# Kernel tuning notes

Measured on AMD Instinct MI355X. Metric: run time of the kernel, lower is better.

The kernel has to match this reference:

```python
import jax, jax.numpy as jnp
import numpy as np

DIM = 384
NUM_HEADS = 6
HEAD_DIM = DIM // NUM_HEADS
SCALE = HEAD_DIM ** -0.5


def setup_inputs() -> dict:
    key = jax.random.key(0)
    k_x, k_wqkv, k_bqkv, k_wp, k_bp = jax.random.split(key, 5)
    B, N, D = 16, 1024, DIM
    s = 0.02
    return {
        "x": jax.random.normal(k_x, (B, N, D), dtype=jnp.float32),
        "w_qkv": jax.random.normal(k_wqkv, (D, 3 * D), dtype=jnp.float32) * s,
        "b_qkv": jax.random.normal(k_bqkv, (3 * D,), dtype=jnp.float32) * s,
        "w_proj": jax.random.normal(k_wp, (D, D), dtype=jnp.float32) * s,
        "b_proj": jax.random.normal(k_bp, (D,), dtype=jnp.float32) * s,
    }


def reference(x, w_qkv, b_qkv, w_proj, b_proj):
    b, n, d = x.shape
    qkv = x @ w_qkv + b_qkv                               # (B, N, 3D)
    qkv = qkv.reshape(b, n, 3, NUM_HEADS, HEAD_DIM)
    qkv = jnp.transpose(qkv, (2, 0, 3, 1, 4))             # (3, B, H, N, hd)
    q, k, v = qkv[0], qkv[1], qkv[2]
    attn = jnp.einsum("bhqd,bhkd->bhqk", q, k) * SCALE    # (B, H, N, N)
    attn = jax.nn.softmax(attn, axis=-1)
    out = jnp.einsum("bhqk,bhkd->bhqd", attn, v)          # (B, H, N, hd)
    out = jnp.transpose(out, (0, 2, 1, 3)).reshape(b, n, d)
    return out @ w_proj + b_proj
```

## Files before the change

kernel.cpp:

```cpp
#include <hip/hip_runtime.h>

typedef __attribute__((ext_vector_type(8))) short short8;
typedef __attribute__((ext_vector_type(4))) float float4_t;
typedef __attribute__((ext_vector_type(4))) unsigned int uint4_t;

#define MFMA16(A, B, C) __builtin_amdgcn_mfma_f32_16x16x32_bf16(A, B, C, 0, 0, 0)

#define QSCALE 0.1803368801111168f

__device__ __forceinline__ unsigned short f2bf(float f) {
  unsigned int u = __builtin_bit_cast(unsigned int, f);
  u += 0x7FFFu + ((u >> 16) & 1u);
  return (unsigned short)(u >> 16);
}

__device__ __forceinline__ void gload16(const unsigned short* g, unsigned short* l) {
  __builtin_amdgcn_global_load_lds(
      (const __attribute__((address_space(1))) unsigned int*)(g),
      (__attribute__((address_space(3))) unsigned int*)(l), 16, 0, 0);
}

__global__ __launch_bounds__(256) void prep(
    const float* __restrict__ x, const float* __restrict__ w_qkv,
    const float* __restrict__ w_proj, unsigned short* __restrict__ xb,
    unsigned short* __restrict__ wqkvT, unsigned short* __restrict__ wprojT) {
  __shared__ unsigned short tile[32][33];
  const int bid = blockIdx.x, tid = threadIdx.x;
  if (bid < 6144) {
    const int i = bid * 256 + tid;
    float4 v = reinterpret_cast<const float4*>(x)[i];
    ushort4 r;
    r.x = f2bf(v.x); r.y = f2bf(v.y); r.z = f2bf(v.z); r.w = f2bf(v.w);
    reinterpret_cast<ushort4*>(xb)[i] = r;
    return;
  }
  const float* w; unsigned short* wT; int E, t;
  if (bid < 6576) { t = bid - 6144; w = w_qkv; wT = wqkvT; E = 1152; }
  else            { t = bid - 6576; w = w_proj; wT = wprojT; E = 384; }
  const int tiles_e = E >> 5;
  const int td = t / tiles_e, te = t - td * tiles_e;
  const int r = tid >> 3, c4 = (tid & 7) * 4;
  float4 v = *reinterpret_cast<const float4*>(&w[(size_t)(td * 32 + r) * E + te * 32 + c4]);
  tile[r][c4 + 0] = f2bf(v.x);
  tile[r][c4 + 1] = f2bf(v.y);
  tile[r][c4 + 2] = f2bf(v.z);
  tile[r][c4 + 3] = f2bf(v.w);
  __syncthreads();
  ushort4 o;
  o.x = tile[c4 + 0][r]; o.y = tile[c4 + 1][r];
  o.z = tile[c4 + 2][r]; o.w = tile[c4 + 3][r];
  *reinterpret_cast<ushort4*>(&wT[(size_t)(te * 32 + r) * 384 + td * 32 + c4]) = o;
}

__global__ __launch_bounds__(256, 3) void gemm_qkv(
    const unsigned short* __restrict__ xb,
    const unsigned short* __restrict__ wT,
    const float* __restrict__ bias,
    unsigned short* __restrict__ qb,
    unsigned short* __restrict__ kb,
    unsigned short* __restrict__ vt) {
  __shared__ alignas(16) char smem[49152];
  const int tid = threadIdx.x;
  const int wg = (blockIdx.x & 7) * 288 + (blockIdx.x >> 3);
  const int bm = wg / 18, bn = wg - bm * 18;
  const int m0 = bm * 128, n0 = bn * 64;
  const int lane = tid & 63, wid = tid >> 6;
  const int lr = lane & 15, lg = lane >> 4;
  const int wm = wid >> 1, wn = wid & 1;
  float4_t acc[4][2] = {};

  const unsigned short* asrc[4];
  const unsigned short* bsrc[2];
  int adst[4], bdst[2];
#pragma unroll
  for (int i = 0; i < 4; ++i) {
    const int idx = tid + i * 256;
    const int r = idx >> 3, c8 = idx & 7;
    asrc[i] = xb + (size_t)(m0 + r) * 384 + (c8 ^ (r & 7)) * 8;
    adst[i] = idx * 16;
  }
#pragma unroll
  for (int i = 0; i < 2; ++i) {
    const int idx = tid + i * 256;
    const int r = idx >> 3, c8 = idx & 7;
    bsrc[i] = wT + (size_t)(n0 + r) * 384 + (c8 ^ (r & 7)) * 8;
    bdst[i] = idx * 16;
  }
  const int rxor = (lr & 7) << 4;

#pragma unroll
  for (int i = 0; i < 4; ++i) gload16(asrc[i], (unsigned short*)(smem + adst[i]));
#pragma unroll
  for (int i = 0; i < 2; ++i) gload16(bsrc[i], (unsigned short*)(smem + 32768 + bdst[i]));
  __syncthreads();

#pragma unroll
  for (int kt = 0; kt < 6; ++kt) {
    const int cur = kt & 1;
    if (kt < 5) {
#pragma unroll
      for (int i = 0; i < 4; ++i)
        gload16(asrc[i] + (kt + 1) * 64,
                (unsigned short*)(smem + (cur ^ 1) * 16384 + adst[i]));
#pragma unroll
      for (int i = 0; i < 2; ++i)
        gload16(bsrc[i] + (kt + 1) * 64,
                (unsigned short*)(smem + 32768 + (cur ^ 1) * 8192 + bdst[i]));
    }
    const char* Ab = smem + cur * 16384;
    const char* Bb = smem + 32768 + cur * 8192;
#pragma unroll
    for (int kk = 0; kk < 2; ++kk) {
      short8 a[4], b[2];
#pragma unroll
      for (int f = 0; f < 4; ++f)
        a[f] = *reinterpret_cast<const short8*>(
            Ab + (wm * 64 + f * 16 + lr) * 128 + ((kk * 64 + lg * 16) ^ rxor));
#pragma unroll
      for (int f = 0; f < 2; ++f)
        b[f] = *reinterpret_cast<const short8*>(
            Bb + (wn * 32 + f * 16 + lr) * 128 + ((kk * 64 + lg * 16) ^ rxor));
      if (bn < 12) {
#pragma unroll
        for (int mf = 0; mf < 4; ++mf)
#pragma unroll
          for (int nf = 0; nf < 2; ++nf)
            acc[mf][nf] = MFMA16(b[nf], a[mf], acc[mf][nf]);
      } else {
#pragma unroll
        for (int mf = 0; mf < 4; ++mf)
#pragma unroll
          for (int nf = 0; nf < 2; ++nf)
            acc[mf][nf] = MFMA16(a[mf], b[nf], acc[mf][nf]);
      }
    }
    __syncthreads();
  }

  if (bn < 12) {
    const int whichk = (bn >= 6);
    unsigned short* dst = whichk ? kb : qb;
    const float sc = whichk ? 1.f : QSCALE;
#pragma unroll
    for (int nf = 0; nf < 2; ++nf) {
      const int e0 = n0 + wn * 32 + nf * 16 + lg * 4;
      const int d0 = e0 - whichk * 384;
      const int h = d0 >> 6, hi0 = d0 & 63;
      const float4 bv4 = *reinterpret_cast<const float4*>(&bias[e0]);
#pragma unroll
      for (int mf = 0; mf < 4; ++mf) {
        const int mm = m0 + wm * 64 + mf * 16 + lr;
        const int b0 = mm >> 10, n_b = mm & 1023;
        const size_t bhh = (size_t)(b0 * 6 + h);
        ushort4 sv;
        sv.x = f2bf((acc[mf][nf][0] + bv4.x) * sc);
        sv.y = f2bf((acc[mf][nf][1] + bv4.y) * sc);
        sv.z = f2bf((acc[mf][nf][2] + bv4.z) * sc);
        sv.w = f2bf((acc[mf][nf][3] + bv4.w) * sc);
        *reinterpret_cast<ushort4*>(&dst[bhh * 65536 + (size_t)n_b * 64 + hi0]) = sv;
      }
    }
  } else {
#pragma unroll
    for (int nf = 0; nf < 2; ++nf) {
      const int e = n0 + wn * 32 + nf * 16 + lr;
      const float bv = bias[e];
      const int d = e - 768;
      const int h = d >> 6, hi = d & 63;
#pragma unroll
      for (int mf = 0; mf < 4; ++mf) {
        const int mm0 = m0 + wm * 64 + mf * 16 + lg * 4;
        const int b0 = mm0 >> 10, n_b = mm0 & 1023;
        const size_t bhh = (size_t)(b0 * 6 + h);
        const int np = (n_b & ~31) | ((n_b & 12) << 1) | ((n_b & 16) >> 2);
        ushort4 sv;
        sv.x = f2bf(acc[mf][nf][0] + bv);
        sv.y = f2bf(acc[mf][nf][1] + bv);
        sv.z = f2bf(acc[mf][nf][2] + bv);
        sv.w = f2bf(acc[mf][nf][3] + bv);
        *reinterpret_cast<ushort4*>(&vt[bhh * 65536 + (size_t)hi * 1024 + np]) = sv;
      }
    }
  }
}

__global__ __launch_bounds__(512, 6) void attn(
    const unsigned short* __restrict__ qb,
    const unsigned short* __restrict__ kb,
    const unsigned short* __restrict__ vt,
    unsigned short* __restrict__ ab) {
  __shared__ alignas(16) char smem[32768];
  const int tid = threadIdx.x;
  const int wg = (blockIdx.x & 7) * 96 + (blockIdx.x >> 3);
  const int bh = wg >> 3, qt = wg & 7;
  const int lane = tid & 63, wid = tid >> 6;
  const int lr = lane & 15, lg = lane >> 4;
  const size_t base = (size_t)bh * 65536;
  const unsigned short* qp = qb + base;
  const unsigned short* kp = kb + base;
  const unsigned short* vp = vt + base;
  const int q0 = qt * 128 + wid * 16;

  short8 aq0 = *reinterpret_cast<const short8*>(&qp[(size_t)(q0 + lr) * 64 + lg * 8]);
  short8 aq1 = *reinterpret_cast<const short8*>(&qp[(size_t)(q0 + lr) * 64 + 32 + lg * 8]);

  const int rr = tid >> 3;
  const int cc = (((tid & 7) * 16) ^ ((rr & 7) << 4)) >> 1;
  const unsigned short* ksrc = kp + rr * 64 + cc;
  const unsigned short* vsrc = vp + rr * 1024 + cc;
  unsigned short* kdst = (unsigned short*)(smem + tid * 16);
  unsigned short* vdst = (unsigned short*)(smem + 16384 + tid * 16);

  const int xr = (lr & 7) << 4;

  float lsum = 0.f;
  float4_t o[4] = {};

  gload16(ksrc, kdst);
  gload16(vsrc, vdst);
  __syncthreads();

  for (int kt = 0; kt < 16; ++kt) {
    const int cur = kt & 1;
    if (kt < 15) {
      const int nb = (cur ^ 1) * 8192;
      gload16(ksrc + (kt + 1) * 4096, (unsigned short*)(smem + nb + tid * 16));
      gload16(vsrc + (kt + 1) * 64, (unsigned short*)(smem + 16384 + nb + tid * 16));
    }
    const char* kbase = smem + cur * 8192;
    const char* vbase = smem + 16384 + cur * 8192;

#pragma unroll
    for (int half = 0; half < 2; ++half) {
      short8 bk00 = *reinterpret_cast<const short8*>(
          kbase + (half * 32 + lr) * 128 + ((lg * 16) ^ xr));
      short8 bk01 = *reinterpret_cast<const short8*>(
          kbase + (half * 32 + lr) * 128 + ((64 + lg * 16) ^ xr));
      short8 bk10 = *reinterpret_cast<const short8*>(
          kbase + (half * 32 + 16 + lr) * 128 + ((lg * 16) ^ xr));
      short8 bk11 = *reinterpret_cast<const short8*>(
          kbase + (half * 32 + 16 + lr) * 128 + ((64 + lg * 16) ^ xr));
      float4_t s0 = {}, s1 = {};
      __builtin_amdgcn_s_setprio(1);
      s0 = MFMA16(bk00, aq0, s0);
      s0 = MFMA16(bk01, aq1, s0);
      s1 = MFMA16(bk10, aq0, s1);
      s1 = MFMA16(bk11, aq1, s1);
      __builtin_amdgcn_s_setprio(0);

      unsigned int dw0, dw1, dw2, dw3;
      {
        const float p0 = __builtin_amdgcn_exp2f(s0[0]);
        const float p1 = __builtin_amdgcn_exp2f(s0[1]);
        const float p2 = __builtin_amdgcn_exp2f(s0[2]);
        const float p3 = __builtin_amdgcn_exp2f(s0[3]);
        asm("v_cvt_pk_bf16_f32 %0, %1, %2" : "=v"(dw0) : "v"(p0), "v"(p1));
        asm("v_cvt_pk_bf16_f32 %0, %1, %2" : "=v"(dw1) : "v"(p2), "v"(p3));
        const float p4 = __builtin_amdgcn_exp2f(s1[0]);
        const float p5 = __builtin_amdgcn_exp2f(s1[1]);
        const float p6 = __builtin_amdgcn_exp2f(s1[2]);
        const float p7 = __builtin_amdgcn_exp2f(s1[3]);
        asm("v_cvt_pk_bf16_f32 %0, %1, %2" : "=v"(dw2) : "v"(p4), "v"(p5));
        asm("v_cvt_pk_bf16_f32 %0, %1, %2" : "=v"(dw3) : "v"(p6), "v"(p7));
      }
      const float t0 = __builtin_bit_cast(float, dw0 << 16) +
                       __builtin_bit_cast(float, dw0 & 0xFFFF0000u);
      const float t1 = __builtin_bit_cast(float, dw1 << 16) +
                       __builtin_bit_cast(float, dw1 & 0xFFFF0000u);
      const float t2 = __builtin_bit_cast(float, dw2 << 16) +
                       __builtin_bit_cast(float, dw2 & 0xFFFF0000u);
      const float t3 = __builtin_bit_cast(float, dw3 << 16) +
                       __builtin_bit_cast(float, dw3 & 0xFFFF0000u);
      lsum += (t0 + t1) + (t2 + t3);

      uint4_t pw;
      pw[0] = dw0; pw[1] = dw1; pw[2] = dw2; pw[3] = dw3;
      const short8 pa = __builtin_bit_cast(short8, pw);
      short8 bv0 = *reinterpret_cast<const short8*>(
          vbase + (0 * 16 + lr) * 128 + ((half * 64 + lg * 16) ^ xr));
      short8 bv1 = *reinterpret_cast<const short8*>(
          vbase + (1 * 16 + lr) * 128 + ((half * 64 + lg * 16) ^ xr));
      short8 bv2 = *reinterpret_cast<const short8*>(
          vbase + (2 * 16 + lr) * 128 + ((half * 64 + lg * 16) ^ xr));
      short8 bv3 = *reinterpret_cast<const short8*>(
          vbase + (3 * 16 + lr) * 128 + ((half * 64 + lg * 16) ^ xr));
      __builtin_amdgcn_s_setprio(1);
      o[0] = MFMA16(pa, bv0, o[0]);
      o[1] = MFMA16(pa, bv1, o[1]);
      o[2] = MFMA16(pa, bv2, o[2]);
      o[3] = MFMA16(pa, bv3, o[3]);
      __builtin_amdgcn_s_setprio(0);
    }
    __syncthreads();
  }

  float t = lsum;
  t += __shfl_xor(t, 16);
  t += __shfl_xor(t, 32);
  const float inv = 1.f / t;

  const int b = bh / 6, h = bh - b * 6;
  float invj[4];
#pragma unroll
  for (int j = 0; j < 4; ++j)
    invj[j] = __shfl(inv, lg * 4 + j);
#pragma unroll
  for (int f = 0; f < 4; ++f)
#pragma unroll
    for (int j = 0; j < 4; ++j) {
      const int q = q0 + lg * 4 + j;
      ab[(size_t)(b * 1024 + q) * 384 + h * 64 + f * 16 + lr] =
          f2bf(o[f][j] * invj[j]);
    }
}

__global__ __launch_bounds__(256, 3) void gemm_proj(
    const unsigned short* __restrict__ ab,
    const unsigned short* __restrict__ wT,
    const float* __restrict__ bias,
    float* __restrict__ out) {
  __shared__ alignas(16) char smem[49152];
  const int tid = threadIdx.x;
  const int wg = (blockIdx.x & 7) * 96 + (blockIdx.x >> 3);
  const int bm = wg / 3, bn = wg - bm * 3;
  const int m0 = bm * 64, n0 = bn * 128;
  const int lane = tid & 63, wid = tid >> 6;
  const int lr = lane & 15, lg = lane >> 4;
  const int wm = wid >> 1, wn = wid & 1;
  float4_t acc[2][4] = {};

  const unsigned short* asrc[2];
  const unsigned short* bsrc[4];
  int adst[2], bdst[4];
#pragma unroll
  for (int i = 0; i < 2; ++i) {
    const int idx = tid + i * 256;
    const int r = idx >> 3, c8 = idx & 7;
    asrc[i] = ab + (size_t)(m0 + r) * 384 + (c8 ^ (r & 7)) * 8;
    adst[i] = idx * 16;
  }
#pragma unroll
  for (int i = 0; i < 4; ++i) {
    const int idx = tid + i * 256;
    const int r = idx >> 3, c8 = idx & 7;
    bsrc[i] = wT + (size_t)(n0 + r) * 384 + (c8 ^ (r & 7)) * 8;
    bdst[i] = idx * 16;
  }
  const int rxor = (lr & 7) << 4;

#pragma unroll
  for (int i = 0; i < 2; ++i) gload16(asrc[i], (unsigned short*)(smem + adst[i]));
#pragma unroll
  for (int i = 0; i < 4; ++i) gload16(bsrc[i], (unsigned short*)(smem + 16384 + bdst[i]));
  __syncthreads();

#pragma unroll
  for (int kt = 0; kt < 6; ++kt) {
    const int cur = kt & 1;
    if (kt < 5) {
#pragma unroll
      for (int i = 0; i < 2; ++i)
        gload16(asrc[i] + (kt + 1) * 64, (unsigned short*)(smem + (cur ^ 1) * 8192 + adst[i]));
#pragma unroll
      for (int i = 0; i < 4; ++i)
        gload16(bsrc[i] + (kt + 1) * 64, (unsigned short*)(smem + 16384 + (cur ^ 1) * 16384 + bdst[i]));
    }
    const char* Ab = smem + cur * 8192;
    const char* Bb = smem + 16384 + cur * 16384;
#pragma unroll
    for (int kk = 0; kk < 2; ++kk) {
      short8 a[2], b[4];
#pragma unroll
      for (int f = 0; f < 2; ++f)
        a[f] = *reinterpret_cast<const short8*>(
            Ab + (wm * 32 + f * 16 + lr) * 128 + ((kk * 64 + lg * 16) ^ rxor));
#pragma unroll
      for (int f = 0; f < 4; ++f)
        b[f] = *reinterpret_cast<const short8*>(
            Bb + (wn * 64 + f * 16 + lr) * 128 + ((kk * 64 + lg * 16) ^ rxor));
#pragma unroll
      for (int mf = 0; mf < 2; ++mf)
#pragma unroll
        for (int nf = 0; nf < 4; ++nf)
          acc[mf][nf] = MFMA16(b[nf], a[mf], acc[mf][nf]);
    }
    __syncthreads();
  }

#pragma unroll
  for (int nf = 0; nf < 4; ++nf) {
    const int e0 = n0 + wn * 64 + nf * 16 + lg * 4;
    const float4 bv4 = *reinterpret_cast<const float4*>(&bias[e0]);
#pragma unroll
    for (int mf = 0; mf < 2; ++mf) {
      const int mm = m0 + wm * 32 + mf * 16 + lr;
      float4 ov;
      ov.x = acc[mf][nf][0] + bv4.x;
      ov.y = acc[mf][nf][1] + bv4.y;
      ov.z = acc[mf][nf][2] + bv4.z;
      ov.w = acc[mf][nf][3] + bv4.w;
      *reinterpret_cast<float4*>(&out[(size_t)mm * 384 + e0]) = ov;
    }
  }
}

extern "C" void kernel_launch(void* const* d_in, const int* in_sizes, int n_in,
                              void* d_out, int out_size, void* d_ws, size_t ws_size,
                              hipStream_t stream) {
  const float* x      = (const float*)d_in[0];
  const float* w_qkv  = (const float*)d_in[1];
  const float* b_qkv  = (const float*)d_in[2];
  const float* w_proj = (const float*)d_in[3];
  const float* b_proj = (const float*)d_in[4];
  float* out = (float*)d_out;

  char* ws = (char*)d_ws;
  unsigned short* xb     = (unsigned short*)(ws);
  unsigned short* wqkvT  = (unsigned short*)(ws + 12582912);
  unsigned short* wprojT = (unsigned short*)(ws + 13467648);
  unsigned short* qb     = (unsigned short*)(ws + 13762560);
  unsigned short* kb     = (unsigned short*)(ws + 26345472);
  unsigned short* vt     = (unsigned short*)(ws + 38928384);
  unsigned short* ab     = xb;

  prep<<<6720, 256, 0, stream>>>(x, w_qkv, w_proj, xb, wqkvT, wprojT);
  gemm_qkv<<<2304, 256, 0, stream>>>(xb, wqkvT, b_qkv, qb, kb, vt);
  attn<<<768, 512, 0, stream>>>(qb, kb, vt, ab);
  gemm_proj<<<768, 256, 0, stream>>>(ab, wprojT, b_proj, out);
}
```

Baseline: 88.34 us.

## Give each attention wave two query tiles so K/V LDS reads are reused

The attention kernel drops from 512 to 256 threads per block, and each wave now processes 32 query rows (two 16-row fragments) instead of 16. The K and V fragments read from LDS are reused across both query fragments, which halves LDS read traffic per unit of MFMA work. Each thread now issues two async global-to-LDS loads per tile instead of one. The cost is more registers per wave (two output accumulators, four Q fragments) and fewer waves per block, which may reduce latency hiding.

```diff
diff --git a/kernel.cpp b/kernel.cpp
--- a/kernel.cpp
+++ b/kernel.cpp
@@ -184,7 +184,7 @@
   }
 }
 
-__global__ __launch_bounds__(512, 6) void attn(
+__global__ __launch_bounds__(256, 3) void attn(
     const unsigned short* __restrict__ qb,
     const unsigned short* __restrict__ kb,
     const unsigned short* __restrict__ vt,
@@ -199,33 +199,49 @@
   const unsigned short* qp = qb + base;
   const unsigned short* kp = kb + base;
   const unsigned short* vp = vt + base;
-  const int q0 = qt * 128 + wid * 16;
-
-  short8 aq0 = *reinterpret_cast<const short8*>(&qp[(size_t)(q0 + lr) * 64 + lg * 8]);
-  short8 aq1 = *reinterpret_cast<const short8*>(&qp[(size_t)(q0 + lr) * 64 + 32 + lg * 8]);
-
-  const int rr = tid >> 3;
-  const int cc = (((tid & 7) * 16) ^ ((rr & 7) << 4)) >> 1;
-  const unsigned short* ksrc = kp + rr * 64 + cc;
-  const unsigned short* vsrc = vp + rr * 1024 + cc;
-  unsigned short* kdst = (unsigned short*)(smem + tid * 16);
-  unsigned short* vdst = (unsigned short*)(smem + 16384 + tid * 16);
-
+  const int q0 = qt * 128 + wid * 32;
+
+  short8 aq[2][2];
+#pragma unroll
+  for (int qf = 0; qf < 2; ++qf)
+#pragma unroll
+    for (int h = 0; h < 2; ++h)
+      aq[qf][h] = *reinterpret_cast<const short8*>(
+          &qp[(size_t)(q0 + qf * 16 + lr) * 64 + h * 32 + lg * 8]);
+
+  const unsigned short* ksrc[2];
+  const unsigned short* vsrc[2];
+  int soff[2];
+#pragma unroll
+  for (int i = 0; i < 2; ++i) {
+    const int idx = tid + i * 256;
+    const int r = idx >> 3, c8 = idx & 7;
+    const int cc = (c8 ^ (r & 7)) * 8;
+    ksrc[i] = kp + r * 64 + cc;
+    vsrc[i] = vp + r * 1024 + cc;
+    soff[i] = idx * 16;
+  }
   const int xr = (lr & 7) << 4;
 
-  float lsum = 0.f;
-  float4_t o[4] = {};
-
-  gload16(ksrc, kdst);
-  gload16(vsrc, vdst);
+  float lsum0 = 0.f, lsum1 = 0.f;
+  float4_t o0[4] = {}, o1[4] = {};
+
+#pragma unroll
+  for (int i = 0; i < 2; ++i) {
+    gload16(ksrc[i], (unsigned short*)(smem + soff[i]));
+    gload16(vsrc[i], (unsigned short*)(smem + 16384 + soff[i]));
+  }
   __syncthreads();
 
   for (int kt = 0; kt < 16; ++kt) {
     const int cur = kt & 1;
     if (kt < 15) {
       const int nb = (cur ^ 1) * 8192;
-      gload16(ksrc + (kt + 1) * 4096, (unsigned short*)(smem + nb + tid * 16));
-      gload16(vsrc + (kt + 1) * 64, (unsigned short*)(smem + 16384 + nb + tid * 16));
+#pragma unroll
+      for (int i = 0; i < 2; ++i) {
+        gload16(ksrc[i] + (kt + 1) * 4096, (unsigned short*)(smem + nb + soff[i]));
+        gload16(vsrc[i] + (kt + 1) * 64, (unsigned short*)(smem + 16384 + nb + soff[i]));
+      }
     }
     const char* kbase = smem + cur * 8192;
     const char* vbase = smem + 16384 + cur * 8192;
@@ -240,42 +256,6 @@
           kbase + (half * 32 + 16 + lr) * 128 + ((lg * 16) ^ xr));
       short8 bk11 = *reinterpret_cast<const short8*>(
           kbase + (half * 32 + 16 + lr) * 128 + ((64 + lg * 16) ^ xr));
-      float4_t s0 = {}, s1 = {};
-      __builtin_amdgcn_s_setprio(1);
-      s0 = MFMA16(bk00, aq0, s0);
-      s0 = MFMA16(bk01, aq1, s0);
-      s1 = MFMA16(bk10, aq0, s1);
-      s1 = MFMA16(bk11, aq1, s1);
-      __builtin_amdgcn_s_setprio(0);
-
-      unsigned int dw0, dw1, dw2, dw3;
-      {
-        const float p0 = __builtin_amdgcn_exp2f(s0[0]);
-        const float p1 = __builtin_amdgcn_exp2f(s0[1]);
-        const float p2 = __builtin_amdgcn_exp2f(s0[2]);
-        const float p3 = __builtin_amdgcn_exp2f(s0[3]);
-        asm("v_cvt_pk_bf16_f32 %0, %1, %2" : "=v"(dw0) : "v"(p0), "v"(p1));
-        asm("v_cvt_pk_bf16_f32 %0, %1, %2" : "=v"(dw1) : "v"(p2), "v"(p3));
-        const float p4 = __builtin_amdgcn_exp2f(s1[0]);
-        const float p5 = __builtin_amdgcn_exp2f(s1[1]);
-        const float p6 = __builtin_amdgcn_exp2f(s1[2]);
-        const float p7 = __builtin_amdgcn_exp2f(s1[3]);
-        asm("v_cvt_pk_bf16_f32 %0, %1, %2" : "=v"(dw2) : "v"(p4), "v"(p5));
-        asm("v_cvt_pk_bf16_f32 %0, %1, %2" : "=v"(dw3) : "v"(p6), "v"(p7));
-      }
-      const float t0 = __builtin_bit_cast(float, dw0 << 16) +
-                       __builtin_bit_cast(float, dw0 & 0xFFFF0000u);
-      const float t1 = __builtin_bit_cast(float, dw1 << 16) +
-                       __builtin_bit_cast(float, dw1 & 0xFFFF0000u);
-      const float t2 = __builtin_bit_cast(float, dw2 << 16) +
-                       __builtin_bit_cast(float, dw2 & 0xFFFF0000u);
-      const float t3 = __builtin_bit_cast(float, dw3 << 16) +
-                       __builtin_bit_cast(float, dw3 & 0xFFFF0000u);
-      lsum += (t0 + t1) + (t2 + t3);
-
-      uint4_t pw;
-      pw[0] = dw0; pw[1] = dw1; pw[2] = dw2; pw[3] = dw3;
-      const short8 pa = __builtin_bit_cast(short8, pw);
       short8 bv0 = *reinterpret_cast<const short8*>(
           vbase + (0 * 16 + lr) * 128 + ((half * 64 + lg * 16) ^ xr));
       short8 bv1 = *reinterpret_cast<const short8*>(
@@ -284,34 +264,84 @@
           vbase + (2 * 16 + lr) * 128 + ((half * 64 + lg * 16) ^ xr));
       short8 bv3 = *reinterpret_cast<const short8*>(
           vbase + (3 * 16 + lr) * 128 + ((half * 64 + lg * 16) ^ xr));
-      __builtin_amdgcn_s_setprio(1);
-      o[0] = MFMA16(pa, bv0, o[0]);
-      o[1] = MFMA16(pa, bv1, o[1]);
-      o[2] = MFMA16(pa, bv2, o[2]);
-      o[3] = MFMA16(pa, bv3, o[3]);
-      __builtin_amdgcn_s_setprio(0);
+
+#pragma unroll
+      for (int qf = 0; qf < 2; ++qf) {
+        float4_t s0 = {}, s1 = {};
+        __builtin_amdgcn_s_setprio(1);
+        s0 = MFMA16(bk00, aq[qf][0], s0);
+        s0 = MFMA16(bk01, aq[qf][1], s0);
+        s1 = MFMA16(bk10, aq[qf][0], s1);
+        s1 = MFMA16(bk11, aq[qf][1], s1);
+        __builtin_amdgcn_s_setprio(0);
+
+        unsigned int dw0, dw1, dw2, dw3;
+        {
+          const float p0 = __builtin_amdgcn_exp2f(s0[0]);
+          const float p1 = __builtin_amdgcn_exp2f(s0[1]);
+          const float p2 = __builtin_amdgcn_exp2f(s0[2]);
+          const float p3 = __builtin_amdgcn_exp2f(s0[3]);
+          asm("v_cvt_pk_bf16_f32 %0, %1, %2" : "=v"(dw0) : "v"(p0), "v"(p1));
+          asm("v_cvt_pk_bf16_f32 %0, %1, %2" : "=v"(dw1) : "v"(p2), "v"(p3));
+          const float p4 = __builtin_amdgcn_exp2f(s1[0]);
+          const float p5 = __builtin_amdgcn_exp2f(s1[1]);
+          const float p6 = __builtin_amdgcn_exp2f(s1[2]);
+          const float p7 = __builtin_amdgcn_exp2f(s1[3]);
+          asm("v_cvt_pk_bf16_f32 %0, %1, %2" : "=v"(dw2) : "v"(p4), "v"(p5));
+          asm("v_cvt_pk_bf16_f32 %0, %1, %2" : "=v"(dw3) : "v"(p6), "v"(p7));
+        }
+        const float t0 = __builtin_bit_cast(float, dw0 << 16) +
+                         __builtin_bit_cast(float, dw0 & 0xFFFF0000u);
+        const float t1 = __builtin_bit_cast(float, dw1 << 16) +
+                         __builtin_bit_cast(float, dw1 & 0xFFFF0000u);
+        const float t2 = __builtin_bit_cast(float, dw2 << 16) +
+                         __builtin_bit_cast(float, dw2 & 0xFFFF0000u);
+        const float t3 = __builtin_bit_cast(float, dw3 << 16) +
+                         __builtin_bit_cast(float, dw3 & 0xFFFF0000u);
+        if (qf == 0) lsum0 += (t0 + t1) + (t2 + t3);
+        else         lsum1 += (t0 + t1) + (t2 + t3);
+
+        uint4_t pw;
+        pw[0] = dw0; pw[1] = dw1; pw[2] = dw2; pw[3] = dw3;
+        const short8 pa = __builtin_bit_cast(short8, pw);
+        float4_t* o = (qf == 0) ? o0 : o1;
+        __builtin_amdgcn_s_setprio(1);
+        o[0] = MFMA16(pa, bv0, o[0]);
+        o[1] = MFMA16(pa, bv1, o[1]);
+        o[2] = MFMA16(pa, bv2, o[2]);
+        o[3] = MFMA16(pa, bv3, o[3]);
+        __builtin_amdgcn_s_setprio(0);
+      }
     }
     __syncthreads();
   }
 
-  float t = lsum;
-  t += __shfl_xor(t, 16);
-  t += __shfl_xor(t, 32);
-  const float inv = 1.f / t;
+  float ti0 = lsum0, ti1 = lsum1;
+  ti0 += __shfl_xor(ti0, 16);
+  ti0 += __shfl_xor(ti0, 32);
+  ti1 += __shfl_xor(ti1, 16);
+  ti1 += __shfl_xor(ti1, 32);
+  const float inv0 = 1.f / ti0;
+  const float inv1 = 1.f / ti1;
 
   const int b = bh / 6, h = bh - b * 6;
-  float invj[4];
-#pragma unroll
-  for (int j = 0; j < 4; ++j)
-    invj[j] = __shfl(inv, lg * 4 + j);
-#pragma unroll
-  for (int f = 0; f < 4; ++f)
-#pragma unroll
-    for (int j = 0; j < 4; ++j) {
-      const int q = q0 + lg * 4 + j;
-      ab[(size_t)(b * 1024 + q) * 384 + h * 64 + f * 16 + lr] =
-          f2bf(o[f][j] * invj[j]);
-    }
+#pragma unroll
+  for (int qf = 0; qf < 2; ++qf) {
+    const float4_t* o = (qf == 0) ? o0 : o1;
+    const float inv = (qf == 0) ? inv0 : inv1;
+    float invj[4];
+#pragma unroll
+    for (int j = 0; j < 4; ++j)
+      invj[j] = __shfl(inv, lg * 4 + j);
+#pragma unroll
+    for (int f = 0; f < 4; ++f)
+#pragma unroll
+      for (int j = 0; j < 4; ++j) {
+        const int q = q0 + qf * 16 + lg * 4 + j;
+        ab[(size_t)(b * 1024 + q) * 384 + h * 64 + f * 16 + lr] =
+            f2bf(o[f][j] * invj[j]);
+      }
+  }
 }
 
 __global__ __launch_bounds__(256, 3) void gemm_proj(
@@ -425,6 +455,6 @@
 
   prep<<<6720, 256, 0, stream>>>(x, w_qkv, w_proj, xb, wqkvT, wprojT);
   gemm_qkv<<<2304, 256, 0, stream>>>(xb, wqkvT, b_qkv, qb, kb, vt);
-  attn<<<768, 512, 0, stream>>>(qb, kb, vt, ab);
+  attn<<<768, 256, 0, stream>>>(qb, kb, vt, ab);
   gemm_proj<<<768, 256, 0, stream>>>(ab, wprojT, b_proj, out);
 }
```

Result: faster. 85.92 us (median of 3 runs) (-2.7%).
